# Kernel tuning notes

Hardware: AMD Instinct MI355X
Metric: run time of the kernel (lower is better)

The kernel has to match this reference:

```python
import jax, jax.numpy as jnp
import numpy as np

IN_CH = 512
HID = 1024
N_HEADS = 16
HEAD_DIM = HID // N_HEADS  # 64
BSZ = 1024
LN_EPS = 1e-5


def setup_inputs() -> dict:
    key = jax.random.key(0)
    ks = jax.random.split(key, 8)
    kvb_out = N_HEADS * (2 * HEAD_DIM + 1)
    return {
        "x": jax.random.normal(ks[0], (BSZ, IN_CH), dtype=jnp.float32),
        "W": jax.random.normal(ks[1], (BSZ, N_HEADS * HEAD_DIM * HEAD_DIM), dtype=jnp.float32) * 0.02,
        "w_in": jax.random.normal(ks[2], (HID, IN_CH), dtype=jnp.float32) * (1.0 / np.sqrt(IN_CH)),
        "b_in": jnp.zeros((HID,), dtype=jnp.float32),
        "gamma": jnp.ones((HID,), dtype=jnp.float32),
        "beta": jnp.zeros((HID,), dtype=jnp.float32),
        "w_kvb": jax.random.normal(ks[3], (kvb_out, HID), dtype=jnp.float32) * (1.0 / np.sqrt(HID)),
        "b_kvb": jnp.zeros((kvb_out,), dtype=jnp.float32),
    }


def reference(x, W, w_in, b_in, gamma, beta, w_kvb, b_kvb):
    bsz = x.shape[0]
    # input_proj + LayerNorm
    h = x @ w_in.T + b_in  # [B, HID]
    mu = jnp.mean(h, axis=-1, keepdims=True)
    var = jnp.mean((h - mu) ** 2, axis=-1, keepdims=True)
    h = (h - mu) * jax.lax.rsqrt(var + LN_EPS) * gamma + beta
    # kvb_net
    out = h @ w_kvb.T + b_kvb  # [B, H*(2d+1)]
    out = out.reshape(bsz, N_HEADS, 2 * HEAD_DIM + 1)
    ks_ = out[..., :HEAD_DIM]                    # [B, H, d]
    vs = jnp.tanh(out[..., HEAD_DIM:2 * HEAD_DIM])  # [B, H, d]
    lrs = jax.nn.sigmoid(out[..., 2 * HEAD_DIM:])   # [B, H, 1]
    # Oja removal: ks -= W^T v per head
    W_t = W.reshape(bsz, N_HEADS, HEAD_DIM, HEAD_DIM)
    ks_remove = jnp.einsum("bhij,bhi->bhj", W_t, vs)
    ks_ = ks_ - ks_remove
    ks_ = jax.nn.softmax(ks_, axis=-1) * lrs     # [B, H, d]
    # outer product v k^T per head
    dW = jnp.einsum("bhi,bhj->bhij", vs, ks_)    # [B, H, d, d]
    return dW.reshape(bsz, -1)
```

## Files before the change

### kernel.cpp

```cpp
#include <hip/hip_runtime.h>
#include <hip/hip_bf16.h>
#include <math.h>

#define IN_CH 512
#define HID   1024
#define NH    16
#define HD    64
#define BSZ   1024
#define KVB   2064
#define NPAD  2112
#define LN_EPS 1e-5f

typedef _Float16 f16x8 __attribute__((ext_vector_type(8)));
typedef float f32x4  __attribute__((ext_vector_type(4)));
typedef unsigned short u16;

__device__ inline void split16(float f, u16& hi, u16& lo) {
    _Float16 h = (_Float16)f;
    _Float16 l = (_Float16)(f - (float)h);
    hi = __builtin_bit_cast(u16, h);
    lo = __builtin_bit_cast(u16, l);
}
__device__ inline u16 f2h(float f) {
    _Float16 h = (_Float16)f;
    return __builtin_bit_cast(u16, h);
}

__device__ inline void gload16(const void* g, void* l) {
    __builtin_amdgcn_global_load_lds(
        (const __attribute__((address_space(1))) unsigned int*)g,
        (__attribute__((address_space(3))) unsigned int*)l, 16, 0, 0);
}

#define QX (BSZ * IN_CH / 4)
#define QW (HID * IN_CH / 4)
#define QK (NPAD * HID / 4)
#define QKVALID (KVB * HID / 4)
#define TOTQ (QX + QW + QK)

__global__ __launch_bounds__(256) void cvt_all(const float* __restrict__ x,
                                               const float* __restrict__ w_in,
                                               const float* __restrict__ w_kvb,
                                               u16* __restrict__ xh, u16* __restrict__ xl,
                                               u16* __restrict__ wih,
                                               u16* __restrict__ wkh) {
    long q = (long)blockIdx.x * 256 + threadIdx.x;
    if (q < QX) {
        float4 v = ((const float4*)x)[q];
        float f[4] = {v.x, v.y, v.z, v.w};
        ushort4 hh4, ll4;
        u16 hb[4], lb[4];
        #pragma unroll
        for (int j = 0; j < 4; ++j) split16(f[j], hb[j], lb[j]);
        hh4.x = hb[0]; hh4.y = hb[1]; hh4.z = hb[2]; hh4.w = hb[3];
        ll4.x = lb[0]; ll4.y = lb[1]; ll4.z = lb[2]; ll4.w = lb[3];
        ((ushort4*)xh)[q] = hh4;
        ((ushort4*)xl)[q] = ll4;
    } else if (q < QX + QW) {
        long lq = q - QX;
        float4 v = ((const float4*)w_in)[lq];
        ushort4 hh4;
        hh4.x = f2h(v.x); hh4.y = f2h(v.y); hh4.z = f2h(v.z); hh4.w = f2h(v.w);
        ((ushort4*)wih)[lq] = hh4;
    } else {
        long lq = q - QX - QW;
        float4 v = (lq < QKVALID) ? ((const float4*)w_kvb)[lq]
                                  : make_float4(0.f, 0.f, 0.f, 0.f);
        ushort4 hh4;
        hh4.x = f2h(v.x); hh4.y = f2h(v.y); hh4.z = f2h(v.z); hh4.w = f2h(v.w);
        ((ushort4*)wkh)[lq] = hh4;
    }
}

template<int BM, int BN, int KK>
__global__ __launch_bounds__(256) void gemm_f16(const u16* __restrict__ Ah_g,
                                                const u16* __restrict__ Al_g,
                                                const u16* __restrict__ Bh_g,
                                                const float* __restrict__ bias,
                                                float* __restrict__ C,
                                                int N, int ldc) {
    constexpr int WM = BM / 2, WN = BN / 2, MF = WM / 16, NF = WN / 16;
    constexpr int AU = BM / 16;
    constexpr int U  = 2 * AU + BN / 16;
    __shared__ __align__(16) u16 Ah[2][BM][32];
    __shared__ __align__(16) u16 Al[2][BM][32];
    __shared__ __align__(16) u16 Bh[2][BN][32];

    const int t = threadIdx.x, lane = t & 63, wid = t >> 6;
    const int wm = wid >> 1, wn = wid & 1;
    const int m0 = blockIdx.y * BM, n0 = blockIdx.x * BN;

    f32x4 acc[MF][NF] = {};

    auto stage = [&](int buf, int k0) {
        #pragma unroll
        for (int it = 0; it < U / 4; ++it) {
            int u = it * 4 + wid;
            if (u < AU) {
                int c = u * 64 + lane, row = c >> 2, seg = (c & 3) ^ (row & 3);
                gload16(Ah_g + (size_t)(m0 + row) * KK + k0 + seg * 8,
                        &Ah[buf][u * 16][0]);
            } else if (u < 2 * AU) {
                int uu = u - AU;
                int c = uu * 64 + lane, row = c >> 2, seg = (c & 3) ^ (row & 3);
                gload16(Al_g + (size_t)(m0 + row) * KK + k0 + seg * 8,
                        &Al[buf][uu * 16][0]);
            } else {
                int bu = u - 2 * AU;
                int c = bu * 64 + lane, row = c >> 2, seg = (c & 3) ^ (row & 3);
                gload16(Bh_g + (size_t)(n0 + row) * KK + k0 + seg * 8,
                        &Bh[buf][bu * 16][0]);
            }
        }
    };

    constexpr int KT = KK / 32;
    stage(0, 0);
    __syncthreads();
    int buf = 0;
    for (int kt = 0; kt < KT; ++kt) {
        if (kt + 1 < KT) stage(buf ^ 1, (kt + 1) * 32);

        f16x8 ah[MF], al[MF], bh[NF];
        #pragma unroll
        for (int mf = 0; mf < MF; ++mf) {
            int r = wm * WM + mf * 16 + (lane & 15);
            int c = (lane >> 4) ^ (r & 3);
            ah[mf] = *(const f16x8*)&Ah[buf][r][c * 8];
            al[mf] = *(const f16x8*)&Al[buf][r][c * 8];
        }
        #pragma unroll
        for (int nf = 0; nf < NF; ++nf) {
            int r = wn * WN + nf * 16 + (lane & 15);
            int c = (lane >> 4) ^ (r & 3);
            bh[nf] = *(const f16x8*)&Bh[buf][r][c * 8];
        }
        #pragma unroll
        for (int mf = 0; mf < MF; ++mf)
            #pragma unroll
            for (int nf = 0; nf < NF; ++nf) {
                acc[mf][nf] = __builtin_amdgcn_mfma_f32_16x16x32_f16(ah[mf], bh[nf], acc[mf][nf], 0, 0, 0);
                acc[mf][nf] = __builtin_amdgcn_mfma_f32_16x16x32_f16(al[mf], bh[nf], acc[mf][nf], 0, 0, 0);
            }
        __syncthreads();
        buf ^= 1;
    }

    #pragma unroll
    for (int mf = 0; mf < MF; ++mf)
        #pragma unroll
        for (int nf = 0; nf < NF; ++nf) {
            int col = n0 + wn * WN + nf * 16 + (lane & 15);
            if (col < N) {
                float bb = bias[col];
                #pragma unroll
                for (int r = 0; r < 4; ++r) {
                    int row = m0 + wm * WM + mf * 16 + ((lane >> 4) << 2) + r;
                    C[(size_t)row * ldc + col] = acc[mf][nf][r] + bb;
                }
            }
        }
}

__global__ __launch_bounds__(256) void ln_rows(const float* __restrict__ h,
                                               const float* __restrict__ gamma,
                                               const float* __restrict__ beta,
                                               u16* __restrict__ hh,
                                               u16* __restrict__ hl) {
    const int row = blockIdx.x;
    const int t   = threadIdx.x;
    const float* hr = h + (size_t)row * HID;

    float4 v = *(const float4*)(hr + t * 4);
    float s  = v.x + v.y + v.z + v.w;
    float sq = v.x * v.x + v.y * v.y + v.z * v.z + v.w * v.w;

    #pragma unroll
    for (int off = 1; off < 64; off <<= 1) {
        s  += __shfl_xor(s, off);
        sq += __shfl_xor(sq, off);
    }
    __shared__ float red[8];
    const int wid = t >> 6;
    if ((t & 63) == 0) { red[wid] = s; red[4 + wid] = sq; }
    __syncthreads();
    s  = red[0] + red[1] + red[2] + red[3];
    sq = red[4] + red[5] + red[6] + red[7];

    const float mu  = s * (1.f / HID);
    const float var = sq * (1.f / HID) - mu * mu;
    const float inv = rsqrtf(var + LN_EPS);

    float4 g  = *(const float4*)(gamma + t * 4);
    float4 be = *(const float4*)(beta + t * 4);
    float o[4];
    o[0] = (v.x - mu) * inv * g.x + be.x;
    o[1] = (v.y - mu) * inv * g.y + be.y;
    o[2] = (v.z - mu) * inv * g.z + be.z;
    o[3] = (v.w - mu) * inv * g.w + be.w;

    ushort4 uh, ul;
    u16 hb[4], lb[4];
    #pragma unroll
    for (int j = 0; j < 4; ++j) split16(o[j], hb[j], lb[j]);
    uh.x = hb[0]; uh.y = hb[1]; uh.z = hb[2]; uh.w = hb[3];
    ul.x = lb[0]; ul.y = lb[1]; ul.z = lb[2]; ul.w = lb[3];
    ((ushort4*)(hh + (size_t)row * HID))[t] = uh;
    ((ushort4*)(hl + (size_t)row * HID))[t] = ul;
}

__global__ __launch_bounds__(256) void oja_tail(const float* __restrict__ out2,
                                                const float* __restrict__ W,
                                                float* __restrict__ dW) {
    const int lane = threadIdx.x & 63;
    const int wid  = threadIdx.x >> 6;
    const int pair = blockIdx.x * 4 + wid;
    const int b    = pair >> 4;
    const int head = pair & 15;

    const float* orow = out2 + (size_t)b * KVB + head * (2 * HD + 1);

    const float kin   = orow[lane];
    const float vfull = tanhf(orow[64 + lane]);
    float t3 = 0.f;
    if (lane == 0) t3 = orow[128];
    const float lrl = __shfl(t3, 0);
    const float lr  = 1.f / (1.f + expf(-lrl));

    const int g   = lane >> 4;
    const int c16 = lane & 15;

    const float* wbh = W + (size_t)pair * (HD * HD);

    float rem[4] = {0.f, 0.f, 0.f, 0.f};
    #pragma unroll
    for (int tt = 0; tt < 16; ++tt) {
        const int i = 4 * tt + g;
        const float vsi = __shfl(vfull, i);
        float4 w4 = *(const float4*)(wbh + i * 64 + c16 * 4);
        rem[0] = fmaf(w4.x, vsi, rem[0]);
        rem[1] = fmaf(w4.y, vsi, rem[1]);
        rem[2] = fmaf(w4.z, vsi, rem[2]);
        rem[3] = fmaf(w4.w, vsi, rem[3]);
    }
    #pragma unroll
    for (int q = 0; q < 4; ++q) {
        rem[q] += __shfl_xor(rem[q], 16);
        rem[q] += __shfl_xor(rem[q], 32);
    }

    float L[4];
    #pragma unroll
    for (int q = 0; q < 4; ++q)
        L[q] = __shfl(kin, 4 * c16 + q) - rem[q];

    float mx = fmaxf(fmaxf(L[0], L[1]), fmaxf(L[2], L[3]));
    #pragma unroll
    for (int off = 1; off < 16; off <<= 1)
        mx = fmaxf(mx, __shfl_xor(mx, off));

    float e[4], ssum = 0.f;
    #pragma unroll
    for (int q = 0; q < 4; ++q) { e[q] = expf(L[q] - mx); ssum += e[q]; }
    #pragma unroll
    for (int off = 1; off < 16; off <<= 1)
        ssum += __shfl_xor(ssum, off);

    const float scale = lr / ssum;
    float ks[4];
    #pragma unroll
    for (int q = 0; q < 4; ++q) ks[q] = e[q] * scale;

    float* obh = dW + (size_t)pair * (HD * HD);
    #pragma unroll
    for (int tt = 0; tt < 16; ++tt) {
        const int i = 4 * tt + g;
        const float vsi = __shfl(vfull, i);
        float4 o = make_float4(vsi * ks[0], vsi * ks[1], vsi * ks[2], vsi * ks[3]);
        *(float4*)(obh + i * 64 + c16 * 4) = o;
    }
}

extern "C" void kernel_launch(void* const* d_in, const int* in_sizes, int n_in,
                              void* d_out, int out_size, void* d_ws, size_t ws_size,
                              hipStream_t stream) {
    const float* x     = (const float*)d_in[0];
    const float* W     = (const float*)d_in[1];
    const float* w_in  = (const float*)d_in[2];
    const float* b_in  = (const float*)d_in[3];
    const float* gamma = (const float*)d_in[4];
    const float* beta  = (const float*)d_in[5];
    const float* w_kvb = (const float*)d_in[6];
    const float* b_kvb = (const float*)d_in[7];
    float* dW = (float*)d_out;

    char* p = (char*)d_ws;
    auto carve = [&](size_t bytes) { char* r = p; p += (bytes + 255) & ~(size_t)255; return r; };
    float* h    = (float*)carve((size_t)BSZ * HID * 4);
    float* out2 = (float*)carve((size_t)BSZ * KVB * 4);
    u16* xh  = (u16*)carve((size_t)BSZ * IN_CH * 2);
    u16* xl  = (u16*)carve((size_t)BSZ * IN_CH * 2);
    u16* wih = (u16*)carve((size_t)HID * IN_CH * 2);
    u16* hh  = (u16*)carve((size_t)BSZ * HID * 2);
    u16* hl  = (u16*)carve((size_t)BSZ * HID * 2);
    u16* wkh = (u16*)carve((size_t)NPAD * HID * 2);

    cvt_all<<<TOTQ / 256, 256, 0, stream>>>(x, w_in, w_kvb, xh, xl, wih, wkh);

    gemm_f16<32, 64, IN_CH><<<dim3(HID / 64, BSZ / 32), 256, 0, stream>>>(
        xh, xl, wih, b_in, h, HID, HID);

    ln_rows<<<BSZ, 256, 0, stream>>>(h, gamma, beta, hh, hl);

    gemm_f16<64, 64, HID><<<dim3(NPAD / 64, BSZ / 64), 256, 0, stream>>>(
        hh, hl, wkh, b_kvb, out2, KVB, KVB);

    oja_tail<<<(BSZ * NH) / 4, 256, 0, stream>>>(out2, W, dW);
}
```

Measured before the change: 151.2 us.

## Double GEMM K-tile to 64, add XCD-aware block swizzle, nontemporal tail IO

The GEMM kernel now stages K tiles of 64 instead of 32, with an 8-way XOR-swizzled LDS layout, halving the number of sync/stage iterations. The second GEMM uses a 1D grid remapped so that consecutive blocks on the same XCD share tiles, aiming for better L2 reuse. The Oja tail uses nontemporal loads for W and nontemporal stores for dW to avoid polluting cache with streamed data. LDS use doubles per block, which may reduce occupancy.

```diff
diff --git a/kernel.cpp b/kernel.cpp
--- a/kernel.cpp
+++ b/kernel.cpp
@@ -72,7 +72,7 @@
     }
 }
 
-template<int BM, int BN, int KK>
+template<int BM, int BN, int KK, bool SWZ>
 __global__ __launch_bounds__(256) void gemm_f16(const u16* __restrict__ Ah_g,
                                                 const u16* __restrict__ Al_g,
                                                 const u16* __restrict__ Bh_g,
@@ -80,15 +80,30 @@
                                                 float* __restrict__ C,
                                                 int N, int ldc) {
     constexpr int WM = BM / 2, WN = BN / 2, MF = WM / 16, NF = WN / 16;
-    constexpr int AU = BM / 16;
-    constexpr int U  = 2 * AU + BN / 16;
-    __shared__ __align__(16) u16 Ah[2][BM][32];
-    __shared__ __align__(16) u16 Al[2][BM][32];
-    __shared__ __align__(16) u16 Bh[2][BN][32];
+    constexpr int UA = BM / 8;
+    constexpr int UB = BN / 8;
+    constexpr int U  = 2 * UA + UB;
+    __shared__ __align__(16) u16 Ah[2][BM][64];
+    __shared__ __align__(16) u16 Al[2][BM][64];
+    __shared__ __align__(16) u16 Bh[2][BN][64];
 
     const int t = threadIdx.x, lane = t & 63, wid = t >> 6;
     const int wm = wid >> 1, wn = wid & 1;
-    const int m0 = blockIdx.y * BM, n0 = blockIdx.x * BN;
+
+    int mt, nt;
+    if (SWZ) {
+        int bid = blockIdx.x;
+        int nwg = gridDim.x;
+        int w = (bid & 7) * (nwg >> 3) + (bid >> 3);
+        mt = w & (BSZ / BM - 1);
+        nt = w / (BSZ / BM);
+    } else {
+        nt = blockIdx.x; mt = blockIdx.y;
+    }
+    const int m0 = mt * BM, n0 = nt * BN;
+
+    const int seg = (lane & 7) ^ (lane >> 3);
+    const int r8  = lane >> 3;
 
     f32x4 acc[MF][NF] = {};
 
@@ -96,52 +111,57 @@
         #pragma unroll
         for (int it = 0; it < U / 4; ++it) {
             int u = it * 4 + wid;
-            if (u < AU) {
-                int c = u * 64 + lane, row = c >> 2, seg = (c & 3) ^ (row & 3);
+            if (u < UA) {
+                int row = u * 8 + r8;
                 gload16(Ah_g + (size_t)(m0 + row) * KK + k0 + seg * 8,
-                        &Ah[buf][u * 16][0]);
-            } else if (u < 2 * AU) {
-                int uu = u - AU;
-                int c = uu * 64 + lane, row = c >> 2, seg = (c & 3) ^ (row & 3);
+                        &Ah[buf][u * 8][0]);
+            } else if (u < 2 * UA) {
+                int uu = u - UA;
+                int row = uu * 8 + r8;
                 gload16(Al_g + (size_t)(m0 + row) * KK + k0 + seg * 8,
-                        &Al[buf][uu * 16][0]);
+                        &Al[buf][uu * 8][0]);
             } else {
-                int bu = u - 2 * AU;
-                int c = bu * 64 + lane, row = c >> 2, seg = (c & 3) ^ (row & 3);
+                int bu = u - 2 * UA;
+                int row = bu * 8 + r8;
                 gload16(Bh_g + (size_t)(n0 + row) * KK + k0 + seg * 8,
-                        &Bh[buf][bu * 16][0]);
+                        &Bh[buf][bu * 8][0]);
             }
         }
     };
 
-    constexpr int KT = KK / 32;
+    constexpr int KT = KK / 64;
     stage(0, 0);
     __syncthreads();
     int buf = 0;
     for (int kt = 0; kt < KT; ++kt) {
-        if (kt + 1 < KT) stage(buf ^ 1, (kt + 1) * 32);
-
-        f16x8 ah[MF], al[MF], bh[NF];
-        #pragma unroll
-        for (int mf = 0; mf < MF; ++mf) {
-            int r = wm * WM + mf * 16 + (lane & 15);
-            int c = (lane >> 4) ^ (r & 3);
-            ah[mf] = *(const f16x8*)&Ah[buf][r][c * 8];
-            al[mf] = *(const f16x8*)&Al[buf][r][c * 8];
-        }
-        #pragma unroll
-        for (int nf = 0; nf < NF; ++nf) {
-            int r = wn * WN + nf * 16 + (lane & 15);
-            int c = (lane >> 4) ^ (r & 3);
-            bh[nf] = *(const f16x8*)&Bh[buf][r][c * 8];
-        }
-        #pragma unroll
-        for (int mf = 0; mf < MF; ++mf)
+        if (kt + 1 < KT) stage(buf ^ 1, (kt + 1) * 64);
+
+        f16x8 ah[2][MF], al[2][MF], bh[2][NF];
+        #pragma unroll
+        for (int s = 0; s < 2; ++s) {
+            #pragma unroll
+            for (int mf = 0; mf < MF; ++mf) {
+                int r = wm * WM + mf * 16 + (lane & 15);
+                int pc = ((s << 2) | (lane >> 4)) ^ (r & 7);
+                ah[s][mf] = *(const f16x8*)&Ah[buf][r][pc * 8];
+                al[s][mf] = *(const f16x8*)&Al[buf][r][pc * 8];
+            }
             #pragma unroll
             for (int nf = 0; nf < NF; ++nf) {
-                acc[mf][nf] = __builtin_amdgcn_mfma_f32_16x16x32_f16(ah[mf], bh[nf], acc[mf][nf], 0, 0, 0);
-                acc[mf][nf] = __builtin_amdgcn_mfma_f32_16x16x32_f16(al[mf], bh[nf], acc[mf][nf], 0, 0, 0);
+                int r = wn * WN + nf * 16 + (lane & 15);
+                int pc = ((s << 2) | (lane >> 4)) ^ (r & 7);
+                bh[s][nf] = *(const f16x8*)&Bh[buf][r][pc * 8];
             }
+        }
+        #pragma unroll
+        for (int s = 0; s < 2; ++s)
+            #pragma unroll
+            for (int mf = 0; mf < MF; ++mf)
+                #pragma unroll
+                for (int nf = 0; nf < NF; ++nf) {
+                    acc[mf][nf] = __builtin_amdgcn_mfma_f32_16x16x32_f16(ah[s][mf], bh[s][nf], acc[mf][nf], 0, 0, 0);
+                    acc[mf][nf] = __builtin_amdgcn_mfma_f32_16x16x32_f16(al[s][mf], bh[s][nf], acc[mf][nf], 0, 0, 0);
+                }
         __syncthreads();
         buf ^= 1;
     }
@@ -230,18 +250,18 @@
     const int g   = lane >> 4;
     const int c16 = lane & 15;
 
-    const float* wbh = W + (size_t)pair * (HD * HD);
+    const f32x4* wbh = (const f32x4*)(W + (size_t)pair * (HD * HD));
 
     float rem[4] = {0.f, 0.f, 0.f, 0.f};
     #pragma unroll
     for (int tt = 0; tt < 16; ++tt) {
         const int i = 4 * tt + g;
         const float vsi = __shfl(vfull, i);
-        float4 w4 = *(const float4*)(wbh + i * 64 + c16 * 4);
-        rem[0] = fmaf(w4.x, vsi, rem[0]);
-        rem[1] = fmaf(w4.y, vsi, rem[1]);
-        rem[2] = fmaf(w4.z, vsi, rem[2]);
-        rem[3] = fmaf(w4.w, vsi, rem[3]);
+        f32x4 w4 = __builtin_nontemporal_load(wbh + i * 16 + c16);
+        rem[0] = fmaf(w4[0], vsi, rem[0]);
+        rem[1] = fmaf(w4[1], vsi, rem[1]);
+        rem[2] = fmaf(w4[2], vsi, rem[2]);
+        rem[3] = fmaf(w4[3], vsi, rem[3]);
     }
     #pragma unroll
     for (int q = 0; q < 4; ++q) {
@@ -271,13 +291,15 @@
     #pragma unroll
     for (int q = 0; q < 4; ++q) ks[q] = e[q] * scale;
 
-    float* obh = dW + (size_t)pair * (HD * HD);
+    f32x4* obh = (f32x4*)(dW + (size_t)pair * (HD * HD));
     #pragma unroll
     for (int tt = 0; tt < 16; ++tt) {
         const int i = 4 * tt + g;
         const float vsi = __shfl(vfull, i);
-        float4 o = make_float4(vsi * ks[0], vsi * ks[1], vsi * ks[2], vsi * ks[3]);
-        *(float4*)(obh + i * 64 + c16 * 4) = o;
+        f32x4 o;
+        o[0] = vsi * ks[0]; o[1] = vsi * ks[1];
+        o[2] = vsi * ks[2]; o[3] = vsi * ks[3];
+        __builtin_nontemporal_store(o, obh + i * 16 + c16);
     }
 }
 
@@ -307,12 +329,12 @@
 
     cvt_all<<<TOTQ / 256, 256, 0, stream>>>(x, w_in, w_kvb, xh, xl, wih, wkh);
 
-    gemm_f16<32, 64, IN_CH><<<dim3(HID / 64, BSZ / 32), 256, 0, stream>>>(
+    gemm_f16<32, 64, IN_CH, false><<<dim3(HID / 64, BSZ / 32), 256, 0, stream>>>(
         xh, xl, wih, b_in, h, HID, HID);
 
     ln_rows<<<BSZ, 256, 0, stream>>>(h, gamma, beta, hh, hl);
 
-    gemm_f16<64, 64, HID><<<dim3(NPAD / 64, BSZ / 64), 256, 0, stream>>>(
+    gemm_f16<64, 64, HID, true><<<(NPAD / 64) * (BSZ / 64), 256, 0, stream>>>(
         hh, hl, wkh, b_kvb, out2, KVB, KVB);
 
     oja_tail<<<(BSZ * NH) / 4, 256, 0, stream>>>(out2, W, dW);
```

Result: faster. 137.5 us (-9.1%).
